# Kernel optimization log

Hardware: AMD Instinct MI355X
Metric: run time of the kernel (lower is better)

Reference implementation:

```python
import jax, jax.numpy as jnp
import numpy as np
import math

WH, WW = 8, 8
N = WH * WW            # tokens per window = 64
DIM = 128
H = 4                  # num_heads
HD = DIM // H          # head_dim = 32
B_ = 3072              # num_windows * batch
NW = 192               # windows per image (96/8 * 128/8)
LAMBDA_INIT = 0.8 - 0.6 * math.exp(-0.3 * 0)  # layer_idx = 0 -> 0.2
EPS_RMS = 1e-9


def _polar_input():
    # Polar-coordinate relative positions, as in __init__
    gy, gx = jnp.meshgrid(jnp.arange(WH), jnp.arange(WW), indexing='ij')
    flat = jnp.stack([gy.reshape(-1), gx.reshape(-1)])          # (2, N)
    rel = flat[:, :, None] - flat[:, None, :]                   # (2, N, N)
    dx = rel[1].astype(jnp.float32)
    dy = -rel[0].astype(jnp.float32)
    r = jnp.sqrt(dx * dx + dy * dy + 1e-9)
    theta = jnp.arctan2(dx, dy)
    max_r = math.sqrt((WH - 1) ** 2 + (WW - 1) ** 2)
    return jnp.stack([r / max_r, (theta + math.pi) / (2 * math.pi)], axis=-1)  # (N, N, 2)


def setup_inputs() -> dict:
    key = jax.random.key(0)
    ks = jax.random.split(key, 16)
    s = 0.02
    inp = {}
    inp['x'] = jax.random.normal(ks[0], (B_, N, DIM), jnp.float32)
    inp['mask'] = jnp.zeros((NW, N, N), jnp.float32)
    inp['Wqkv'] = jax.random.normal(ks[1], (3 * DIM, DIM), jnp.float32) * s
    inp['bqkv'] = jnp.zeros((3 * DIM,), jnp.float32)
    inp['Wqkv2'] = jax.random.normal(ks[2], (2 * DIM, DIM), jnp.float32) * s
    inp['bqkv2'] = jnp.zeros((2 * DIM,), jnp.float32)
    inp['Wp1'] = jax.random.normal(ks[3], (64, 2), jnp.float32) * 0.1
    inp['bp1'] = jnp.zeros((64,), jnp.float32)
    inp['Wp2'] = jax.random.normal(ks[4], (H, 64), jnp.float32) * 0.1
    inp['bp2'] = jnp.zeros((H,), jnp.float32)
    inp['lambda_q1'] = jax.random.normal(ks[5], (HD // 2,), jnp.float32) * 0.1
    inp['lambda_k1'] = jax.random.normal(ks[6], (HD // 2,), jnp.float32) * 0.1
    inp['lambda_q2'] = jax.random.normal(ks[7], (HD // 2,), jnp.float32) * 0.1
    inp['lambda_k2'] = jax.random.normal(ks[8], (HD // 2,), jnp.float32) * 0.1
    inp['subln_w'] = jnp.ones((HD,), jnp.float32)
    inp['Wproj'] = jax.random.normal(ks[9], (DIM, DIM), jnp.float32) * s
    inp['bproj'] = jnp.zeros((DIM,), jnp.float32)
    return inp


def reference(x, mask, Wqkv, bqkv, Wqkv2, bqkv2, Wp1, bp1, Wp2, bp2,
              lambda_q1, lambda_k1, lambda_q2, lambda_k2, subln_w, Wproj, bproj):
    scale = HD ** -0.5
    # primary q, k, v
    qkv = (x @ Wqkv.T + bqkv).reshape(B_, N, 3, H, HD).transpose(2, 0, 3, 1, 4)
    q, k, v = qkv[0] * scale, qkv[1], qkv[2]        # (B_, H, N, HD)
    # secondary q2, k2 for differential attention
    qk2 = (x @ Wqkv2.T + bqkv2).reshape(B_, N, 2, H, HD).transpose(2, 0, 3, 1, 4)
    q2, k2 = qk2[0] * scale, qk2[1]

    attn = jnp.einsum('bhnd,bhmd->bhnm', q, k)      # (B_, H, N, N)
    attn2 = jnp.einsum('bhnd,bhmd->bhnm', q2, k2)

    lam = (jnp.exp(jnp.sum(lambda_q1 * lambda_k1))
           - jnp.exp(jnp.sum(lambda_q2 * lambda_k2)) + LAMBDA_INIT)

    # MLP-based polar relative position bias (exact erf GELU, as nn.GELU)
    pin = _polar_input().reshape(-1, 2)
    pb = jax.nn.gelu(pin @ Wp1.T + bp1, approximate=False) @ Wp2.T + bp2
    pb = pb.reshape(N, N, H).transpose(2, 0, 1)     # (H, N, N)

    attn = attn - lam * attn2 + pb[None]
    # window mask (0 / -inf), broadcast over batch and heads
    attn = attn.reshape(B_ // NW, NW, H, N, N) + mask[None, :, None]
    attn = jax.nn.softmax(attn.reshape(B_, H, N, N), axis=-1)

    o = jnp.einsum('bhnm,bhmd->bhnd', attn, v)      # (B_, H, N, HD)
    # post-attention RMSNorm over head_dim, then differential rescale
    o = o * jax.lax.rsqrt(jnp.mean(o * o, axis=-1, keepdims=True) + EPS_RMS) * subln_w
    o = (o * (1.0 - LAMBDA_INIT)).transpose(0, 2, 1, 3).reshape(B_, N, DIM)
    return o @ Wproj.T + bproj
```

## Files before the change

kernel.cpp:

```cpp
#include <hip/hip_runtime.h>
#include <math.h>

typedef __attribute__((ext_vector_type(8))) short bf16x8;
typedef __attribute__((ext_vector_type(4))) float f32x4;

#define NWMASK 192
#define SCALE_Q 0.17677669529663687f

__device__ __forceinline__ unsigned short f2bf(float f) {
  union { float f; unsigned u; } v; v.f = f;
  return (unsigned short)((v.u + 0x7fffu + ((v.u >> 16) & 1u)) >> 16);
}

__device__ __forceinline__ unsigned pkbf(float a, float b) {
#if defined(__has_builtin)
#if __has_builtin(__builtin_amdgcn_cvt_pk_bf16_f32)
  auto r = __builtin_amdgcn_cvt_pk_bf16_f32(a, b);
  union { decltype(r) v; unsigned u; } c; c.v = r; return c.u;
#else
  return (unsigned)f2bf(a) | ((unsigned)f2bf(b) << 16);
#endif
#else
  return (unsigned)f2bf(a) | ((unsigned)f2bf(b) << 16);
#endif
}

__device__ __forceinline__ void pack8s(unsigned short* dst, const float* src) {
  float4 lo = *(const float4*)(src);
  float4 hi = *(const float4*)(src + 4);
  uint4 pk;
  pk.x = pkbf(lo.x, lo.y); pk.y = pkbf(lo.z, lo.w);
  pk.z = pkbf(hi.x, hi.y); pk.w = pkbf(hi.z, hi.w);
  *(uint4*)dst = pk;
}

__global__ void prep_kernel(const float* __restrict__ Wqkv, const float* __restrict__ Wqkv2,
                            const float* __restrict__ Wproj,
                            const float* __restrict__ Wp1, const float* __restrict__ bp1,
                            const float* __restrict__ Wp2, const float* __restrict__ bp2,
                            const float* __restrict__ mask,
                            const float* __restrict__ lq1, const float* __restrict__ lk1,
                            const float* __restrict__ lq2, const float* __restrict__ lk2,
                            unsigned short* __restrict__ Wb, float* __restrict__ pbT,
                            float* __restrict__ maskT, float* __restrict__ lamOut) {
  int bid = blockIdx.x;
  if (bid < 48) {
    int gid = bid * 256 + threadIdx.x;
    int l15 = gid & 15, quad = (gid >> 4) & 3, ks = (gid >> 6) & 3, ft = gid >> 8;
    int row = ft * 16 + l15;
    const float* src = (row < 384) ? (Wqkv + (size_t)row * 128)
                     : (row < 640) ? (Wqkv2 + (size_t)(row - 384) * 128)
                                   : (Wproj + (size_t)(row - 640) * 128);
    pack8s(Wb + (size_t)gid * 8, src + ks * 32 + quad * 8);
  } else if (bid < 64) {
    int idx = (bid - 48) * 256 + threadIdx.x;
    int i = idx >> 6, j = idx & 63;
    float dx = (float)((i & 7) - (j & 7));
    float dy = -(float)((i >> 3) - (j >> 3));
    float r = sqrtf(dx*dx + dy*dy + 1e-9f);
    float theta = atan2f(dx, dy);
    float p0 = r * (1.0f / 9.899494936611665f);
    float p1 = (theta + 3.14159265358979323846f) * (1.0f / 6.283185307179586f);
    float a0 = 0.f, a1 = 0.f, a2 = 0.f, a3 = 0.f;
    for (int f = 0; f < 64; ++f) {
      float hpre = p0 * Wp1[2*f] + p1 * Wp1[2*f+1] + bp1[f];
      float g = 0.5f * hpre * (1.0f + erff(hpre * 0.70710678118654752f));
      a0 += Wp2[f]       * g;
      a1 += Wp2[64 + f]  * g;
      a2 += Wp2[128 + f] * g;
      a3 += Wp2[192 + f] * g;
    }
    int o = j * 64 + i;
    pbT[o]          = a0 + bp2[0];
    pbT[4096 + o]   = a1 + bp2[1];
    pbT[8192 + o]   = a2 + bp2[2];
    pbT[12288 + o]  = a3 + bp2[3];
    if (bid == 48 && threadIdx.x == 0) {
      float s1 = 0.f, s2 = 0.f;
      for (int k = 0; k < 16; ++k) { s1 += lq1[k]*lk1[k]; s2 += lq2[k]*lk2[k]; }
      lamOut[0] = expf(s1) - expf(s2) + 0.2f;
    }
  } else {
    __shared__ float tile[64][65];
    int wm = bid - 64;
    const float* src = mask + (size_t)wm * 4096;
#pragma unroll
    for (int u = 0; u < 4; ++u) {
      int o = u * 1024 + threadIdx.x * 4;
      float4 v = *(const float4*)(src + o);
      int r = o >> 6, c = o & 63;
      tile[r][c] = v.x; tile[r][c+1] = v.y; tile[r][c+2] = v.z; tile[r][c+3] = v.w;
    }
    __syncthreads();
    float* dst = maskT + (size_t)wm * 4096;
#pragma unroll
    for (int u = 0; u < 4; ++u) {
      int o = u * 1024 + threadIdx.x * 4;
      int c = o >> 6, r = o & 63;
      float4 v;
      v.x = tile[r][c]; v.y = tile[r+1][c]; v.z = tile[r+2][c]; v.w = tile[r+3][c];
      *(float4*)(dst + o) = v;
    }
  }
}

__global__ __launch_bounds__(512, 6)
void fused_win(const float* __restrict__ x, const unsigned short* __restrict__ Wb,
               const float* __restrict__ bqkv, const float* __restrict__ bqkv2,
               const float* __restrict__ lamBuf,
               const float* __restrict__ subln, const float* __restrict__ bproj,
               const float* __restrict__ pbT, const float* __restrict__ maskT,
               float* __restrict__ out) {
  __shared__ unsigned short smem[24576];

  const int b = blockIdx.x;
  const int t = threadIdx.x;
  const int w = t >> 6;
  const int h = w >> 1;
  const int m = w & 1;
  const int lane = t & 63;
  const int l15 = lane & 15;
  const int quad = lane >> 4;
  const int Rb = m * 32;
  const f32x4 zero4 = (f32x4){0.f, 0.f, 0.f, 0.f};
  const float lam = lamBuf[0];

  {
    const float* xg = x + (size_t)b * 8192;
#pragma unroll
    for (int u = 0; u < 2; ++u) {
      int id = u * 512 + t;
      int r = id >> 4, c16 = id & 15;
      pack8s(&smem[r * 128 + ((c16 ^ (r & 7)) * 8)], xg + r * 128 + c16 * 8);
    }
  }
  __syncthreads();

  unsigned short* QB = smem + 8192 + h * 4096;
  unsigned short* KB = QB + 2048;
  unsigned short* PB = QB;
  unsigned short* VT = smem + h * 2048;

  auto ldXB = [&](int mi, int ks) -> bf16x8 {
    int row = Rb + mi * 16 + l15;
    return *(const bf16x8*)(&smem[row * 128 + (((ks * 4 + quad) ^ (l15 & 7)) * 8)]);
  };
  auto ldWbF = [&](int ft, int ks) -> bf16x8 {
    return *(const bf16x8*)(Wb + ((((size_t)ft * 4 + ks) * 4 + quad) * 16 + l15) * 8);
  };

  auto proj2h = [&](int ft0, int ft1, f32x4 (&acc)[2][2]) {
#pragma unroll
    for (int mi = 0; mi < 2; ++mi) { acc[mi][0] = zero4; acc[mi][1] = zero4; }
#pragma unroll
    for (int ks = 0; ks < 4; ++ks) {
      bf16x8 w0 = ldWbF(ft0, ks), w1 = ldWbF(ft1, ks);
      bf16x8 xa[2];
#pragma unroll
      for (int mi = 0; mi < 2; ++mi) xa[mi] = ldXB(mi, ks);
      __builtin_amdgcn_s_setprio(1);
#pragma unroll
      for (int mi = 0; mi < 2; ++mi) {
        acc[mi][0] = __builtin_amdgcn_mfma_f32_16x16x32_bf16(xa[mi], w0, acc[mi][0], 0, 0, 0);
        acc[mi][1] = __builtin_amdgcn_mfma_f32_16x16x32_bf16(xa[mi], w1, acc[mi][1], 0, 0, 0);
      }
      __builtin_amdgcn_s_setprio(0);
    }
  };
  auto storeM32 = [&](unsigned short* buf, f32x4 (&acc)[2][2], const float* bias, float sc) {
#pragma unroll
    for (int nj = 0; nj < 2; ++nj) {
      int c32 = nj * 16 + l15;
      float bv = bias[c32];
      int g = c32 >> 3, c7 = c32 & 7;
#pragma unroll
      for (int mi = 0; mi < 2; ++mi) {
        f32x4 a = acc[mi][nj];
        unsigned p01 = pkbf((a[0] + bv) * sc, (a[1] + bv) * sc);
        unsigned p23 = pkbf((a[2] + bv) * sc, (a[3] + bv) * sc);
        int r0 = Rb + mi * 16 + quad * 4;
        buf[(r0+0) * 32 + ((g ^ ((r0+0) & 3)) * 8) + c7] = (unsigned short)p01;
        buf[(r0+1) * 32 + ((g ^ ((r0+1) & 3)) * 8) + c7] = (unsigned short)(p01 >> 16);
        buf[(r0+2) * 32 + ((g ^ ((r0+2) & 3)) * 8) + c7] = (unsigned short)p23;
        buf[(r0+3) * 32 + ((g ^ ((r0+3) & 3)) * 8) + c7] = (unsigned short)(p23 >> 16);
      }
    }
  };
  auto qkAll = [&](f32x4 (&S)[2][4], bool seed) {
    bf16x8 qa[2], kb[4];
#pragma unroll
    for (int mi = 0; mi < 2; ++mi) {
      int row = Rb + mi * 16 + l15;
      qa[mi] = *(const bf16x8*)(&QB[row * 32 + ((quad ^ (l15 & 3)) * 8)]);
    }
#pragma unroll
    for (int ni = 0; ni < 4; ++ni) {
      int row = ni * 16 + l15;
      kb[ni] = *(const bf16x8*)(&KB[row * 32 + ((quad ^ (l15 & 3)) * 8)]);
    }
    const float* pbh = pbT + h * 4096;
    const float* mkh = maskT + (size_t)(b % NWMASK) * 4096;
    __builtin_amdgcn_s_setprio(1);
#pragma unroll
    for (int mi = 0; mi < 2; ++mi)
#pragma unroll
      for (int ni = 0; ni < 4; ++ni) {
        f32x4 c;
        if (seed) {
          int off = (ni * 16 + l15) * 64 + Rb + mi * 16 + quad * 4;
          float4 p4 = *(const float4*)(pbh + off);
          float4 m4 = *(const float4*)(mkh + off);
          c[0] = p4.x + m4.x; c[1] = p4.y + m4.y;
          c[2] = p4.z + m4.z; c[3] = p4.w + m4.w;
        } else c = S[mi][ni];
        S[mi][ni] = __builtin_amdgcn_mfma_f32_16x16x32_bf16(qa[mi], kb[ni], c, 0, 0, 0);
      }
    __builtin_amdgcn_s_setprio(0);
  };

  f32x4 S[2][4];
  {
    f32x4 acc[2][2];
    proj2h(24 + 2*h, 25 + 2*h, acc);
    storeM32(QB, acc, bqkv2 + h*32, -lam * SCALE_Q);
    proj2h(32 + 2*h, 33 + 2*h, acc);
    storeM32(KB, acc, bqkv2 + 128 + h*32, 1.0f);
  }
  __syncthreads();
  qkAll(S, true);
  __syncthreads();
  {
    f32x4 acc[2][2];
    proj2h(2*h, 1 + 2*h, acc);
    storeM32(QB, acc, bqkv + h*32, SCALE_Q);
    proj2h(8 + 2*h, 9 + 2*h, acc);
    storeM32(KB, acc, bqkv + 128 + h*32, 1.0f);
  }
  __syncthreads();
  qkAll(S, false);

  unsigned pe01[2][4], pe23[2][4];
#pragma unroll
  for (int mi = 0; mi < 2; ++mi)
#pragma unroll
    for (int reg = 0; reg < 4; ++reg) {
      pe01[mi][reg] = pkbf(__expf(S[mi][0][reg]), __expf(S[mi][1][reg]));
      pe23[mi][reg] = pkbf(__expf(S[mi][2][reg]), __expf(S[mi][3][reg]));
    }
  __syncthreads();
#pragma unroll
  for (int mi = 0; mi < 2; ++mi)
#pragma unroll
    for (int reg = 0; reg < 4; ++reg) {
      int row = Rb + mi * 16 + quad * 4 + reg;
      unsigned short* prow = PB + row * 64;
      int sw = row & 7;
      unsigned v01 = pe01[mi][reg], v23 = pe23[mi][reg];
      prow[(((l15 >> 3) + 0) ^ sw) * 8 + (l15 & 7)] = (unsigned short)v01;
      prow[(((l15 >> 3) + 2) ^ sw) * 8 + (l15 & 7)] = (unsigned short)(v01 >> 16);
      prow[(((l15 >> 3) + 4) ^ sw) * 8 + (l15 & 7)] = (unsigned short)v23;
      prow[(((l15 >> 3) + 6) ^ sw) * 8 + (l15 & 7)] = (unsigned short)(v23 >> 16);
    }

  f32x4 av[2][2];
  proj2h(16 + 2*h, 17 + 2*h, av);
  __syncthreads();
  {
    const float* vbias = bqkv + 256 + h * 32;
#pragma unroll
    for (int nd = 0; nd < 2; ++nd) {
      int d = nd * 16 + l15;
      float bv = vbias[d];
#pragma unroll
      for (int mi = 0; mi < 2; ++mi) {
        int tok = Rb + mi * 16 + quad * 4;
        uint2 pk;
        pk.x = pkbf(av[mi][nd][0] + bv, av[mi][nd][1] + bv);
        pk.y = pkbf(av[mi][nd][2] + bv, av[mi][nd][3] + bv);
        *(uint2*)(&VT[d * 64 + (((tok >> 3) ^ (d & 7)) * 8) + (tok & 7)]) = pk;
      }
    }
  }
  __syncthreads();

  float ov0[2][4], ov1[2][4];
  {
    f32x4 O[2][2];
#pragma unroll
    for (int mi = 0; mi < 2; ++mi) { O[mi][0] = zero4; O[mi][1] = zero4; }
#pragma unroll
    for (int kc = 0; kc < 2; ++kc) {
      bf16x8 pa[2], vb[2];
#pragma unroll
      for (int mi = 0; mi < 2; ++mi) {
        int row = Rb + mi * 16 + l15;
        pa[mi] = *(const bf16x8*)(&PB[row * 64 + (((kc * 4 + quad) ^ (row & 7)) * 8)]);
      }
#pragma unroll
      for (int nd = 0; nd < 2; ++nd) {
        int d = nd * 16 + l15;
        vb[nd] = *(const bf16x8*)(&VT[d * 64 + (((kc * 4 + quad) ^ (d & 7)) * 8)]);
      }
      __builtin_amdgcn_s_setprio(1);
#pragma unroll
      for (int mi = 0; mi < 2; ++mi) {
        O[mi][0] = __builtin_amdgcn_mfma_f32_16x16x32_bf16(pa[mi], vb[0], O[mi][0], 0, 0, 0);
        O[mi][1] = __builtin_amdgcn_mfma_f32_16x16x32_bf16(pa[mi], vb[1], O[mi][1], 0, 0, 0);
      }
      __builtin_amdgcn_s_setprio(0);
    }
    float sw0 = subln[l15] * 0.8f;
    float sw1 = subln[16 + l15] * 0.8f;
#pragma unroll
    for (int mi = 0; mi < 2; ++mi)
#pragma unroll
      for (int reg = 0; reg < 4; ++reg) {
        float a0 = O[mi][0][reg], a1 = O[mi][1][reg];
        float ss = a0 * a0 + a1 * a1;
        ss += __shfl_xor(ss, 1);
        ss += __shfl_xor(ss, 2);
        ss += __shfl_xor(ss, 4);
        ss += __shfl_xor(ss, 8);
        float rs = 1.0f / sqrtf(ss * (1.0f / 32.0f));
        ov0[mi][reg] = a0 * rs * sw0;
        ov1[mi][reg] = a1 * rs * sw1;
      }
  }
  __syncthreads();

  {
    unsigned short* OB = smem + 8192;
    int c0 = h * 32 + l15, c1 = h * 32 + 16 + l15;
#pragma unroll
    for (int mi = 0; mi < 2; ++mi)
#pragma unroll
      for (int reg = 0; reg < 4; ++reg) {
        int row = Rb + mi * 16 + quad * 4 + reg;
        unsigned short* orow = OB + row * 128;
        unsigned p = pkbf(ov0[mi][reg], ov1[mi][reg]);
        orow[(((c0 >> 3) ^ (row & 7)) * 8) + (c0 & 7)] = (unsigned short)p;
        orow[(((c1 >> 3) ^ (row & 7)) * 8) + (c1 & 7)] = (unsigned short)(p >> 16);
      }
  }
  __syncthreads();

  {
    unsigned short* OB = smem + 8192;
    f32x4 po[2][2];
#pragma unroll
    for (int mi = 0; mi < 2; ++mi) { po[mi][0] = zero4; po[mi][1] = zero4; }
#pragma unroll
    for (int ks = 0; ks < 4; ++ks) {
      bf16x8 oa[2];
#pragma unroll
      for (int mi = 0; mi < 2; ++mi) {
        int row = Rb + mi * 16 + l15;
        oa[mi] = *(const bf16x8*)(&OB[row * 128 + (((ks * 4 + quad) ^ (l15 & 7)) * 8)]);
      }
      bf16x8 w0 = ldWbF(40 + 2*h, ks), w1 = ldWbF(41 + 2*h, ks);
      __builtin_amdgcn_s_setprio(1);
#pragma unroll
      for (int mi = 0; mi < 2; ++mi) {
        po[mi][0] = __builtin_amdgcn_mfma_f32_16x16x32_bf16(oa[mi], w0, po[mi][0], 0, 0, 0);
        po[mi][1] = __builtin_amdgcn_mfma_f32_16x16x32_bf16(oa[mi], w1, po[mi][1], 0, 0, 0);
      }
      __builtin_amdgcn_s_setprio(0);
    }
    float* og = out + (size_t)b * 8192;
#pragma unroll
    for (int nt = 0; nt < 2; ++nt) {
      int col = h * 32 + nt * 16 + l15;
      float bp = bproj[col];
#pragma unroll
      for (int mi = 0; mi < 2; ++mi)
#pragma unroll
        for (int reg = 0; reg < 4; ++reg)
          og[(size_t)(Rb + mi * 16 + quad * 4 + reg) * 128 + col] = po[mi][nt][reg] + bp;
    }
  }
}

extern "C" void kernel_launch(void* const* d_in, const int* in_sizes, int n_in,
                              void* d_out, int out_size, void* d_ws, size_t ws_size,
                              hipStream_t stream) {
  (void)in_sizes; (void)n_in; (void)out_size; (void)ws_size;
  const float* x     = (const float*)d_in[0];
  const float* mask  = (const float*)d_in[1];
  const float* Wqkv  = (const float*)d_in[2];
  const float* bqkv  = (const float*)d_in[3];
  const float* Wqkv2 = (const float*)d_in[4];
  const float* bqkv2 = (const float*)d_in[5];
  const float* Wp1   = (const float*)d_in[6];
  const float* bp1   = (const float*)d_in[7];
  const float* Wp2   = (const float*)d_in[8];
  const float* bp2   = (const float*)d_in[9];
  const float* lq1   = (const float*)d_in[10];
  const float* lk1   = (const float*)d_in[11];
  const float* lq2   = (const float*)d_in[12];
  const float* lk2   = (const float*)d_in[13];
  const float* subln = (const float*)d_in[14];
  const float* Wproj = (const float*)d_in[15];
  const float* bproj = (const float*)d_in[16];
  float* out = (float*)d_out;

  unsigned short* Wb = (unsigned short*)d_ws;
  float* lamBuf = (float*)((char*)d_ws + 200704);
  float* pbT   = (float*)((char*)d_ws + 262144);
  float* maskT = (float*)((char*)d_ws + 327680);

  hipLaunchKernelGGL(prep_kernel, dim3(256), dim3(256), 0, stream,
                     Wqkv, Wqkv2, Wproj, Wp1, bp1, Wp2, bp2, mask,
                     lq1, lk1, lq2, lk2, Wb, pbT, maskT, lamBuf);
  hipLaunchKernelGGL(fused_win, dim3(3072), dim3(512), 0, stream,
                     x, Wb, bqkv, bqkv2, lamBuf, subln, bproj,
                     pbT, maskT, out);
}
```

Measured before the change: 324.5 us.

## Compute full K/V per wave to drop block-wide barriers in attention

Each wave now projects K and V for all 64 tokens of its head rather than only its half, and writes them into a per-head LDS region. Q and P move to a per-wave private buffer, which removes several __syncthreads between the QK, softmax and PV stages. The cost is doubled K/V projection MFMA work per head and a larger LDS footprint (80KB vs 48KB), which cuts the number of resident blocks per CU. Launch bounds drop from 6 to 4 to match.

```diff
diff --git a/kernel.cpp b/kernel.cpp
--- a/kernel.cpp
+++ b/kernel.cpp
@@ -104,14 +104,14 @@
   }
 }
 
-__global__ __launch_bounds__(512, 6)
+__global__ __launch_bounds__(512, 4)
 void fused_win(const float* __restrict__ x, const unsigned short* __restrict__ Wb,
                const float* __restrict__ bqkv, const float* __restrict__ bqkv2,
                const float* __restrict__ lamBuf,
                const float* __restrict__ subln, const float* __restrict__ bproj,
                const float* __restrict__ pbT, const float* __restrict__ maskT,
                float* __restrict__ out) {
-  __shared__ unsigned short smem[24576];
+  __shared__ unsigned short smem[40960];
 
   const int b = blockIdx.x;
   const int t = threadIdx.x;
@@ -136,20 +136,25 @@
   }
   __syncthreads();
 
-  unsigned short* QB = smem + 8192 + h * 4096;
-  unsigned short* KB = QB + 2048;
-  unsigned short* PB = QB;
-  unsigned short* VT = smem + h * 2048;
-
-  auto ldXB = [&](int mi, int ks) -> bf16x8 {
+  unsigned short* HB = smem + 8192 + h * 8192;
+  unsigned short* KB = HB;
+  unsigned short* VT = HB + 2048;
+  unsigned short* QB = HB + 4096 + m * 2048;
+  unsigned short* PW = QB;
+
+  auto ldXBo = [&](int mi, int ks) -> bf16x8 {
     int row = Rb + mi * 16 + l15;
     return *(const bf16x8*)(&smem[row * 128 + (((ks * 4 + quad) ^ (l15 & 7)) * 8)]);
   };
+  auto ldXBf = [&](int mi, int ks) -> bf16x8 {
+    int row = mi * 16 + l15;
+    return *(const bf16x8*)(&smem[row * 128 + (((ks * 4 + quad) ^ (l15 & 7)) * 8)]);
+  };
   auto ldWbF = [&](int ft, int ks) -> bf16x8 {
     return *(const bf16x8*)(Wb + ((((size_t)ft * 4 + ks) * 4 + quad) * 16 + l15) * 8);
   };
 
-  auto proj2h = [&](int ft0, int ft1, f32x4 (&acc)[2][2]) {
+  auto projOwn = [&](int ft0, int ft1, f32x4 (&acc)[2][2]) {
 #pragma unroll
     for (int mi = 0; mi < 2; ++mi) { acc[mi][0] = zero4; acc[mi][1] = zero4; }
 #pragma unroll
@@ -157,7 +162,7 @@
       bf16x8 w0 = ldWbF(ft0, ks), w1 = ldWbF(ft1, ks);
       bf16x8 xa[2];
 #pragma unroll
-      for (int mi = 0; mi < 2; ++mi) xa[mi] = ldXB(mi, ks);
+      for (int mi = 0; mi < 2; ++mi) xa[mi] = ldXBo(mi, ks);
       __builtin_amdgcn_s_setprio(1);
 #pragma unroll
       for (int mi = 0; mi < 2; ++mi) {
@@ -167,7 +172,25 @@
       __builtin_amdgcn_s_setprio(0);
     }
   };
-  auto storeM32 = [&](unsigned short* buf, f32x4 (&acc)[2][2], const float* bias, float sc) {
+  auto projFull = [&](int ft0, int ft1, f32x4 (&acc)[4][2]) {
+#pragma unroll
+    for (int mi = 0; mi < 4; ++mi) { acc[mi][0] = zero4; acc[mi][1] = zero4; }
+#pragma unroll
+    for (int ks = 0; ks < 4; ++ks) {
+      bf16x8 w0 = ldWbF(ft0, ks), w1 = ldWbF(ft1, ks);
+      bf16x8 xa[4];
+#pragma unroll
+      for (int mi = 0; mi < 4; ++mi) xa[mi] = ldXBf(mi, ks);
+      __builtin_amdgcn_s_setprio(1);
+#pragma unroll
+      for (int mi = 0; mi < 4; ++mi) {
+        acc[mi][0] = __builtin_amdgcn_mfma_f32_16x16x32_bf16(xa[mi], w0, acc[mi][0], 0, 0, 0);
+        acc[mi][1] = __builtin_amdgcn_mfma_f32_16x16x32_bf16(xa[mi], w1, acc[mi][1], 0, 0, 0);
+      }
+      __builtin_amdgcn_s_setprio(0);
+    }
+  };
+  auto storeQ = [&](f32x4 (&acc)[2][2], const float* bias, float sc) {
 #pragma unroll
     for (int nj = 0; nj < 2; ++nj) {
       int c32 = nj * 16 + l15;
@@ -178,11 +201,30 @@
         f32x4 a = acc[mi][nj];
         unsigned p01 = pkbf((a[0] + bv) * sc, (a[1] + bv) * sc);
         unsigned p23 = pkbf((a[2] + bv) * sc, (a[3] + bv) * sc);
-        int r0 = Rb + mi * 16 + quad * 4;
-        buf[(r0+0) * 32 + ((g ^ ((r0+0) & 3)) * 8) + c7] = (unsigned short)p01;
-        buf[(r0+1) * 32 + ((g ^ ((r0+1) & 3)) * 8) + c7] = (unsigned short)(p01 >> 16);
-        buf[(r0+2) * 32 + ((g ^ ((r0+2) & 3)) * 8) + c7] = (unsigned short)p23;
-        buf[(r0+3) * 32 + ((g ^ ((r0+3) & 3)) * 8) + c7] = (unsigned short)(p23 >> 16);
+        int r0 = mi * 16 + quad * 4;
+        QB[(r0+0) * 32 + ((g ^ ((r0+0) & 3)) * 8) + c7] = (unsigned short)p01;
+        QB[(r0+1) * 32 + ((g ^ ((r0+1) & 3)) * 8) + c7] = (unsigned short)(p01 >> 16);
+        QB[(r0+2) * 32 + ((g ^ ((r0+2) & 3)) * 8) + c7] = (unsigned short)p23;
+        QB[(r0+3) * 32 + ((g ^ ((r0+3) & 3)) * 8) + c7] = (unsigned short)(p23 >> 16);
+      }
+    }
+  };
+  auto storeK = [&](f32x4 (&acc)[4][2], const float* bias) {
+#pragma unroll
+    for (int nj = 0; nj < 2; ++nj) {
+      int c32 = nj * 16 + l15;
+      float bv = bias[c32];
+      int g = c32 >> 3, c7 = c32 & 7;
+#pragma unroll
+      for (int mi = 0; mi < 4; ++mi) {
+        f32x4 a = acc[mi][nj];
+        unsigned p01 = pkbf(a[0] + bv, a[1] + bv);
+        unsigned p23 = pkbf(a[2] + bv, a[3] + bv);
+        int r0 = mi * 16 + quad * 4;
+        KB[(r0+0) * 32 + ((g ^ ((r0+0) & 3)) * 8) + c7] = (unsigned short)p01;
+        KB[(r0+1) * 32 + ((g ^ ((r0+1) & 3)) * 8) + c7] = (unsigned short)(p01 >> 16);
+        KB[(r0+2) * 32 + ((g ^ ((r0+2) & 3)) * 8) + c7] = (unsigned short)p23;
+        KB[(r0+3) * 32 + ((g ^ ((r0+3) & 3)) * 8) + c7] = (unsigned short)(p23 >> 16);
       }
     }
   };
@@ -190,7 +232,7 @@
     bf16x8 qa[2], kb[4];
 #pragma unroll
     for (int mi = 0; mi < 2; ++mi) {
-      int row = Rb + mi * 16 + l15;
+      int row = mi * 16 + l15;
       qa[mi] = *(const bf16x8*)(&QB[row * 32 + ((quad ^ (l15 & 3)) * 8)]);
     }
 #pragma unroll
@@ -220,24 +262,24 @@
 
   f32x4 S[2][4];
   {
-    f32x4 acc[2][2];
-    proj2h(24 + 2*h, 25 + 2*h, acc);
-    storeM32(QB, acc, bqkv2 + h*32, -lam * SCALE_Q);
-    proj2h(32 + 2*h, 33 + 2*h, acc);
-    storeM32(KB, acc, bqkv2 + 128 + h*32, 1.0f);
-  }
+    f32x4 accq[2][2];
+    projOwn(24 + 2*h, 25 + 2*h, accq);
+    storeQ(accq, bqkv2 + h*32, -lam * SCALE_Q);
+    f32x4 acck[4][2];
+    projFull(32 + 2*h, 33 + 2*h, acck);
+    storeK(acck, bqkv2 + 128 + h*32);
+    qkAll(S, true);
+  }
+  f32x4 accq[2][2];
+  projOwn(2*h, 1 + 2*h, accq);
+  storeQ(accq, bqkv + h*32, SCALE_Q);
   __syncthreads();
-  qkAll(S, true);
-  __syncthreads();
-  {
-    f32x4 acc[2][2];
-    proj2h(2*h, 1 + 2*h, acc);
-    storeM32(QB, acc, bqkv + h*32, SCALE_Q);
-    proj2h(8 + 2*h, 9 + 2*h, acc);
-    storeM32(KB, acc, bqkv + 128 + h*32, 1.0f);
-  }
-  __syncthreads();
-  qkAll(S, false);
+  {
+    f32x4 acck[4][2];
+    projFull(8 + 2*h, 9 + 2*h, acck);
+    storeK(acck, bqkv + 128 + h*32);
+    qkAll(S, false);
+  }
 
   unsigned pe01[2][4], pe23[2][4];
 #pragma unroll
@@ -247,13 +289,12 @@
       pe01[mi][reg] = pkbf(__expf(S[mi][0][reg]), __expf(S[mi][1][reg]));
       pe23[mi][reg] = pkbf(__expf(S[mi][2][reg]), __expf(S[mi][3][reg]));
     }
-  __syncthreads();
 #pragma unroll
   for (int mi = 0; mi < 2; ++mi)
 #pragma unroll
     for (int reg = 0; reg < 4; ++reg) {
-      int row = Rb + mi * 16 + quad * 4 + reg;
-      unsigned short* prow = PB + row * 64;
+      int row = mi * 16 + quad * 4 + reg;
+      unsigned short* prow = PW + row * 64;
       int sw = row & 7;
       unsigned v01 = pe01[mi][reg], v23 = pe23[mi][reg];
       prow[(((l15 >> 3) + 0) ^ sw) * 8 + (l15 & 7)] = (unsigned short)v01;
@@ -262,9 +303,8 @@
       prow[(((l15 >> 3) + 6) ^ sw) * 8 + (l15 & 7)] = (unsigned short)(v23 >> 16);
     }
 
-  f32x4 av[2][2];
-  proj2h(16 + 2*h, 17 + 2*h, av);
-  __syncthreads();
+  f32x4 av[4][2];
+  projFull(16 + 2*h, 17 + 2*h, av);
   {
     const float* vbias = bqkv + 256 + h * 32;
 #pragma unroll
@@ -272,8 +312,8 @@
       int d = nd * 16 + l15;
       float bv = vbias[d];
 #pragma unroll
-      for (int mi = 0; mi < 2; ++mi) {
-        int tok = Rb + mi * 16 + quad * 4;
+      for (int mi = 0; mi < 4; ++mi) {
+        int tok = mi * 16 + quad * 4;
         uint2 pk;
         pk.x = pkbf(av[mi][nd][0] + bv, av[mi][nd][1] + bv);
         pk.y = pkbf(av[mi][nd][2] + bv, av[mi][nd][3] + bv);
@@ -281,7 +321,6 @@
       }
     }
   }
-  __syncthreads();
 
   float ov0[2][4], ov1[2][4];
   {
@@ -293,8 +332,8 @@
       bf16x8 pa[2], vb[2];
 #pragma unroll
       for (int mi = 0; mi < 2; ++mi) {
-        int row = Rb + mi * 16 + l15;
-        pa[mi] = *(const bf16x8*)(&PB[row * 64 + (((kc * 4 + quad) ^ (row & 7)) * 8)]);
+        int row = mi * 16 + l15;
+        pa[mi] = *(const bf16x8*)(&PW[row * 64 + (((kc * 4 + quad) ^ (row & 7)) * 8)]);
       }
 #pragma unroll
       for (int nd = 0; nd < 2; ++nd) {
@@ -329,14 +368,13 @@
   __syncthreads();
 
   {
-    unsigned short* OB = smem + 8192;
     int c0 = h * 32 + l15, c1 = h * 32 + 16 + l15;
 #pragma unroll
     for (int mi = 0; mi < 2; ++mi)
 #pragma unroll
       for (int reg = 0; reg < 4; ++reg) {
         int row = Rb + mi * 16 + quad * 4 + reg;
-        unsigned short* orow = OB + row * 128;
+        unsigned short* orow = smem + row * 128;
         unsigned p = pkbf(ov0[mi][reg], ov1[mi][reg]);
         orow[(((c0 >> 3) ^ (row & 7)) * 8) + (c0 & 7)] = (unsigned short)p;
         orow[(((c1 >> 3) ^ (row & 7)) * 8) + (c1 & 7)] = (unsigned short)(p >> 16);
@@ -345,7 +383,6 @@
   __syncthreads();
 
   {
-    unsigned short* OB = smem + 8192;
     f32x4 po[2][2];
 #pragma unroll
     for (int mi = 0; mi < 2; ++mi) { po[mi][0] = zero4; po[mi][1] = zero4; }
@@ -355,7 +392,7 @@
 #pragma unroll
       for (int mi = 0; mi < 2; ++mi) {
         int row = Rb + mi * 16 + l15;
-        oa[mi] = *(const bf16x8*)(&OB[row * 128 + (((ks * 4 + quad) ^ (l15 & 7)) * 8)]);
+        oa[mi] = *(const bf16x8*)(&smem[row * 128 + (((ks * 4 + quad) ^ (l15 & 7)) * 8)]);
       }
       bf16x8 w0 = ldWbF(40 + 2*h, ks), w1 = ldWbF(41 + 2*h, ks);
       __builtin_amdgcn_s_setprio(1);
```

New measurement: 346.3 us. +6.7%, slower.
